# Kernel optimization log

Hardware: AMD Instinct MI355X
Metric: run time of the kernel (lower is better)

The kernel has to match this reference:

```python
import jax, jax.numpy as jnp
import numpy as np

NUM_TRAITS = 5
NUM_MODALITIES = 3
K = 8
EPS = 1e-08


def setup_inputs() -> dict:
    key = jax.random.key(0)
    k1, k2, k3, k4 = jax.random.split(key, 4)
    labeled_embeddings = jax.random.normal(k1, (20000, NUM_MODALITIES, 256), dtype=jnp.float32)
    labeled_traits = jax.random.uniform(k2, (20000, NUM_TRAITS), dtype=jnp.float32)
    unlabeled_embeddings = jax.random.normal(k3, (2048, NUM_MODALITIES, 256), dtype=jnp.float32)
    trait_modality_logits = jax.random.normal(k4, (NUM_TRAITS, NUM_MODALITIES), dtype=jnp.float32)
    return {
        'labeled_embeddings': labeled_embeddings,
        'labeled_traits': labeled_traits,
        'unlabeled_embeddings': unlabeled_embeddings,
        'trait_modality_logits': trait_modality_logits,
    }


def reference(labeled_embeddings, labeled_traits, unlabeled_embeddings, trait_modality_logits):
    # L2-normalize along feature dim (eps added to norm, matching torch code)
    lab_norm = labeled_embeddings / (jnp.linalg.norm(labeled_embeddings, axis=-1, keepdims=True) + EPS)
    unl_norm = unlabeled_embeddings / (jnp.linalg.norm(unlabeled_embeddings, axis=-1, keepdims=True) + EPS)

    # per-modality cosine similarity: [U, M, L]
    modality_sim = jnp.einsum('umd,lmd->uml', unl_norm, lab_norm)

    # per-trait modality weights and weighted similarity: [U, T, L]
    modality_weights = jax.nn.softmax(trait_modality_logits, axis=-1)  # [T, M]
    combined_sim = jnp.einsum('tm,uml->utl', modality_weights, modality_sim)

    # top-k neighbors per (query, trait)
    _, neighbor_indices = jax.lax.top_k(combined_sim, K)  # [U, T, K]

    # gather modality embeddings for neighbors: [U, T, K, M, D]
    neighbor_embeddings = labeled_embeddings[neighbor_indices]

    # gather the trait value corresponding to each trait head: [U, T, K]
    trait_ids = jnp.arange(NUM_TRAITS)[None, :, None]  # [1, T, 1]
    neighbor_traits = labeled_traits[neighbor_indices, trait_ids]

    return neighbor_embeddings, neighbor_traits, neighbor_indices.astype(jnp.int64)
```

## Files before the change

### kernel.cpp

```cpp
#include <hip/hip_runtime.h>
#include <hip/hip_bf16.h>
#include <math.h>

#define L_CNT 20000
#define U_CNT 2048
#define M_CNT 3
#define D_CNT 256
#define KTOT  768
#define T_CNT 5
#define K_OUT 8
#define KC    16
#define LP    20096
#define LROWS (L_CNT*M_CNT)
#define UROWS (U_CNT*M_CNT)
#define CHUNKS 313
#define CPAD   320

typedef unsigned short ushort_t;
typedef unsigned int uint_t;
typedef __attribute__((ext_vector_type(8))) short bf16x8;
typedef __attribute__((ext_vector_type(4))) float f32x4;

__device__ inline double dshfl_xor(double v, int m){
    long long x = __double_as_longlong(v);
    int lo = (int)(x & 0xffffffffLL);
    int hi = (int)(((unsigned long long)x) >> 32);
    lo = __shfl_xor(lo, m, 64);
    hi = __shfl_xor(hi, m, 64);
    return __longlong_as_double(((long long)hi << 32) | (long long)(unsigned int)lo);
}
__device__ inline unsigned short f2bf(float f){
    unsigned int u = __float_as_uint(f);
    u = (u + 0x7fffu + ((u >> 16) & 1u)) >> 16;
    return (unsigned short)u;
}
__device__ __forceinline__ void gload16(const void* g, void* l){
    __builtin_amdgcn_global_load_lds(
        (const __attribute__((address_space(1))) unsigned int*)g,
        (__attribute__((address_space(3))) unsigned int*)l, 16, 0, 0);
}
__device__ __forceinline__ float h2f(ushort_t h){
    _Float16 x; __builtin_memcpy(&x, &h, 2); return (float)x;
}
__device__ __forceinline__ ushort_t f2key(float f){
    _Float16 hv = (_Float16)f;
    ushort_t b; __builtin_memcpy(&b, &hv, 2);
    ushort_t mask = (ushort_t)(0x8000u | (((short)b >> 15) & 0x7FFF));
    return (ushort_t)(b ^ mask);
}
__device__ __forceinline__ ushort_t get16(const uint4& v, int e){
    uint_t w = (e < 2) ? v.x : (e < 4) ? v.y : (e < 6) ? v.z : v.w;
    return (ushort_t)((e & 1) ? (w >> 16) : (w & 0xFFFFu));
}
__device__ __forceinline__ float comb3(float w0, float w1, float w2, float a, float b, float c){
    return fmaf(w2, c, fmaf(w1, b, w0*a));
}
__device__ __forceinline__ void radix_find(uint_t hist[4][256], uint_t* h1, uint_t* h2,
    int tid, uint_t addBase, uint_t kc, uint_t* shB, uint_t* shAbove)
{
    h1[tid] = hist[0][tid]+hist[1][tid]+hist[2][tid]+hist[3][tid];
    uint_t* src = h1; uint_t* dst = h2;
    for (int st=1; st<256; st<<=1){
        __syncthreads();
        dst[tid] = src[tid] + ((tid+st < 256) ? src[tid+st] : 0u);
        uint_t* tt = src; src = dst; dst = tt;
    }
    __syncthreads();
    uint_t ge = src[tid] + addBase;
    uint_t gt = ((tid < 255) ? src[tid+1] : 0u) + addBase;
    if (ge >= kc && gt < kc){ *shB = (uint_t)tid; *shAbove = gt; }
    __syncthreads();
}

__global__ void weights_kernel(const float* __restrict__ logits,
                               float* __restrict__ w32, double* __restrict__ w64){
    int t = threadIdx.x;
    if (t < T_CNT){
        float a = logits[t*M_CNT+0], b = logits[t*M_CNT+1], c = logits[t*M_CNT+2];
        float mx = fmaxf(a, fmaxf(b, c));
        float e0 = expf(a-mx), e1 = expf(b-mx), e2 = expf(c-mx);
        float s = e0+e1+e2;
        w32[t*M_CNT+0] = e0/s; w32[t*M_CNT+1] = e1/s; w32[t*M_CNT+2] = e2/s;
        double da=(double)a, db=(double)b, dc=(double)c;
        double dmx = fmax(da, fmax(db, dc));
        double f0 = exp(da-dmx), f1 = exp(db-dmx), f2 = exp(dc-dmx);
        double ds = f0+f1+f2;
        w64[t*M_CNT+0] = f0/ds; w64[t*M_CNT+1] = f1/ds; w64[t*M_CNT+2] = f2/ds;
    }
}

__global__ __launch_bounds__(256) void prep_kernel(const float* __restrict__ lab,
    const float* __restrict__ unl, double* __restrict__ invL64, double* __restrict__ invU64,
    ushort_t* __restrict__ labN, ushort_t* __restrict__ unlN){
    const int NROW = LROWS + UROWS;
    int row = blockIdx.x*4 + (threadIdx.x >> 6);
    int lane = threadIdx.x & 63;
    if (row >= NROW) return;
    bool isLab = row < LROWS;
    const float* p = isLab ? (lab + (size_t)row*D_CNT) : (unl + (size_t)(row-LROWS)*D_CNT);
    float4 a = ((const float4*)p)[lane];
    double sS = (double)a.x*a.x + (double)a.y*a.y + (double)a.z*a.z + (double)a.w*a.w;
#pragma unroll
    for (int m=1;m<64;m<<=1) sS += dshfl_xor(sS, m);
    double inv = 1.0/(sqrt(sS) + 1e-8);
    if (lane == 0){
        if (isLab) invL64[row] = inv;
        else invU64[row-LROWS] = inv;
    }
    float sc = (float)inv;
    ushort4 o;
    o.x = f2bf(a.x*sc); o.y = f2bf(a.y*sc); o.z = f2bf(a.z*sc); o.w = f2bf(a.w*sc);
    ushort_t* dst = isLab ? (labN + (size_t)row*D_CNT) : (unlN + (size_t)(row-LROWS)*D_CNT);
    *(ushort4*)&dst[lane*4] = o;
}

__global__ __launch_bounds__(256) void sim_kernel(
    const ushort_t* __restrict__ labN, const ushort_t* __restrict__ unlN,
    ushort_t* __restrict__ slabp)
{
    __shared__ ushort_t sA[128][64];
    __shared__ ushort_t sB[128][64];
    __shared__ float    sT[64][132];

    const int tid  = threadIdx.x;
    const int lane = tid & 63;
    const int w    = tid >> 6;
    const int wu = w >> 1, wl = w & 1;
    const int fr = lane & 15, fg = lane >> 4;

    const int uB = blockIdx.x * 128;
    const int l0 = blockIdx.y * 128;

    const int sr   = lane >> 3;
    const int scol = ((lane & 7) ^ sr) * 8;
    const ushort_t* pA[4]; const ushort_t* pB[4];
    ushort_t* dA[4]; ushort_t* dB[4];
#pragma unroll
    for (int g=0; g<4; g++){
        int ar = uB + g*32 + w*8 + sr;
        pA[g] = unlN + (size_t)ar*KTOT + scol;
        dA[g] = &sA[g*32 + w*8][0];
        int br = l0 + g*32 + w*8 + sr; if (br > L_CNT-1) br = L_CNT-1;
        pB[g] = labN + (size_t)br*KTOT + scol;
        dB[g] = &sB[g*32 + w*8][0];
    }

    int aoff[4][2], boff[4][2];
#pragma unroll
    for (int i=0;i<4;i++)
#pragma unroll
        for (int ks=0;ks<2;ks++){
            int sw = ((ks*4 + fg) ^ (fr & 7)) * 16;
            aoff[i][ks] = (wu*64 + i*16 + fr)*128 + sw;
            boff[i][ks] = (wl*64 + i*16 + fr)*128 + sw;
        }

#pragma unroll
    for (int m=0; m<M_CNT; m++){
        f32x4 acc[4][4];
#pragma unroll
        for (int i=0;i<4;i++)
#pragma unroll
            for (int j=0;j<4;j++) acc[i][j] = (f32x4){0.f,0.f,0.f,0.f};

#pragma unroll
        for (int kb=0; kb<4; kb++){
            const int koff = (m*4 + kb) * 64;
            __syncthreads();
#pragma unroll
            for (int g=0; g<4; g++){
                gload16(pA[g] + koff, dA[g]);
                gload16(pB[g] + koff, dB[g]);
            }
            __syncthreads();
#pragma unroll
            for (int ks=0; ks<2; ks++){
                bf16x8 af[4], bf[4];
#pragma unroll
                for (int i=0;i<4;i++) af[i] = *(const bf16x8*)((const char*)sA + aoff[i][ks]);
#pragma unroll
                for (int j=0;j<4;j++) bf[j] = *(const bf16x8*)((const char*)sB + boff[j][ks]);
#pragma unroll
                for (int i=0;i<4;i++)
#pragma unroll
                    for (int j=0;j<4;j++)
                        acc[i][j] = __builtin_amdgcn_mfma_f32_16x16x32_bf16(af[i], bf[j], acc[i][j], 0, 0, 0);
            }
        }
#pragma unroll
        for (int half=0; half<2; half++){
            __syncthreads();
            if (wu == half){
#pragma unroll
                for (int i=0;i<4;i++)
#pragma unroll
                    for (int j=0;j<4;j++)
#pragma unroll
                        for (int r=0;r<4;r++)
                            sT[i*16 + fg*4 + r][wl*64 + j*16 + fr] = acc[i][j][r];
            }
            __syncthreads();
#pragma unroll
            for (int it=0; it<4; it++){
                int row = it*16 + (tid >> 4);
                int c0  = (tid & 15) * 8;
                ushort_t h[8];
#pragma unroll
                for (int e=0;e<8;e++){
                    _Float16 hv = (_Float16)sT[row][c0 + e];
                    __builtin_memcpy(&h[e], &hv, 2);
                }
                size_t base = ((size_t)(uB + half*64 + row)*M_CNT + m)*LP + l0 + c0;
                *(uint4*)&slabp[base] = *(const uint4*)h;
            }
        }
        __syncthreads();
    }
}

__global__ __launch_bounds__(256) void chunkmax_kernel(
    const ushort_t* __restrict__ slabp, const float* __restrict__ w32,
    ushort_t* __restrict__ chunkMax)
{
    __shared__ ushort_t cmax[T_CNT][CPAD];
    const int tid = threadIdx.x;
    const int u = blockIdx.x;

    float w[T_CNT][3];
#pragma unroll
    for (int t=0;t<T_CNT;t++)
#pragma unroll
        for (int m=0;m<3;m++) w[t][m] = w32[t*3+m];

    const uint4* p0 = (const uint4*)(slabp + ((size_t)u*M_CNT + 0)*LP);
    const uint4* p1 = (const uint4*)(slabp + ((size_t)u*M_CNT + 1)*LP);
    const uint4* p2 = (const uint4*)(slabp + ((size_t)u*M_CNT + 2)*LP);

    for (int i=tid; i<T_CNT*CPAD; i+=256) ((ushort_t*)cmax)[i] = 0;
    __syncthreads();

    for (int i=tid; i<2504; i+=256){
        uint_t km[T_CNT] = {0,0,0,0,0};
        if (i < 2500){
            uint4 x = p0[i], y = p1[i], z = p2[i];
            float a[8], b[8], c[8];
#pragma unroll
            for (int e=0;e<8;e++){
                a[e] = h2f(get16(x,e)); b[e] = h2f(get16(y,e)); c[e] = h2f(get16(z,e));
            }
#pragma unroll
            for (int t=0;t<T_CNT;t++){
                uint_t m = 0;
#pragma unroll
                for (int e=0;e<8;e++){
                    uint_t k = f2key(comb3(w[t][0],w[t][1],w[t][2], a[e],b[e],c[e]));
                    m = (k > m) ? k : m;
                }
                km[t] = m;
            }
        }
#pragma unroll
        for (int t=0;t<T_CNT;t++){
            uint_t k = km[t], o;
            o = __shfl_xor((int)k, 1, 64); k = ((uint_t)o > k) ? (uint_t)o : k;
            o = __shfl_xor((int)k, 2, 64); k = ((uint_t)o > k) ? (uint_t)o : k;
            o = __shfl_xor((int)k, 4, 64); k = ((uint_t)o > k) ? (uint_t)o : k;
            if ((tid & 7) == 0) cmax[t][i>>3] = (ushort_t)k;
        }
    }
    __syncthreads();
    for (int i=tid; i<T_CNT*CPAD; i+=256){
        int t = i / CPAD, c = i % CPAD;
        chunkMax[((size_t)u*T_CNT + t)*CPAD + c] = cmax[t][c];
    }
}

__global__ __launch_bounds__(256) void select2_kernel(
    const ushort_t* __restrict__ slabp, const ushort_t* __restrict__ chunkMax,
    const float* __restrict__ w32, int* __restrict__ candIdx)
{
    __shared__ ushort_t mxs[CPAD];
    __shared__ ushort_t cand[CPAD];
    __shared__ uint_t hist[4][256];
    __shared__ uint_t h1[256], h2[256];
    __shared__ uint_t shB, shAbove, shNc, shCtr0, shCtr1;
    __shared__ int bufc[KC];

    const int tid = threadIdx.x, wid = tid >> 6;
    const int u = blockIdx.x, t = blockIdx.y;
    const float w0 = w32[t*3+0], w1 = w32[t*3+1], w2 = w32[t*3+2];
    const ushort_t* s0 = slabp + ((size_t)u*M_CNT + 0)*LP;
    const ushort_t* s1 = slabp + ((size_t)u*M_CNT + 1)*LP;
    const ushort_t* s2 = slabp + ((size_t)u*M_CNT + 2)*LP;
    const ushort_t* cm = chunkMax + ((size_t)u*T_CNT + t)*CPAD;

    for (int i=tid; i<CPAD; i+=256) mxs[i] = (i < CHUNKS) ? cm[i] : (ushort_t)0;
    hist[0][tid]=0; hist[1][tid]=0; hist[2][tid]=0; hist[3][tid]=0;
    if (tid == 0){ shNc = 0; shCtr0 = 0; shCtr1 = 0; }
    __syncthreads();

    for (int i=tid; i<CHUNKS; i+=256) atomicAdd(&hist[wid][mxs[i] >> 8], 1u);
    __syncthreads();
    radix_find(hist, h1, h2, tid, 0u, KC, &shB, &shAbove);
    const uint_t MB = shB, mAb = shAbove;
    hist[0][tid]=0; hist[1][tid]=0; hist[2][tid]=0; hist[3][tid]=0;
    __syncthreads();
    for (int i=tid; i<CHUNKS; i+=256){
        uint_t k = mxs[i];
        if ((k >> 8) == MB) atomicAdd(&hist[wid][k & 0xFFu], 1u);
    }
    __syncthreads();
    radix_find(hist, h1, h2, tid, mAb, KC, &shB, &shAbove);
    const uint_t tau = (MB << 8) | shB;
    hist[0][tid]=0; hist[1][tid]=0; hist[2][tid]=0; hist[3][tid]=0;
    __syncthreads();

    for (int i=tid; i<CHUNKS; i+=256)
        if ((uint_t)mxs[i] >= tau) cand[atomicAdd(&shNc, 1u)] = (ushort_t)i;
    __syncthreads();
    const int NE = (int)shNc * 64;

    for (int j=tid; j<NE; j+=256){
        int l = (int)cand[j>>6]*64 + (j & 63);
        if (l < L_CNT){
            uint_t k = f2key(comb3(w0,w1,w2, h2f(s0[l]), h2f(s1[l]), h2f(s2[l])));
            atomicAdd(&hist[wid][k >> 8], 1u);
        }
    }
    __syncthreads();
    radix_find(hist, h1, h2, tid, 0u, KC, &shB, &shAbove);
    const uint_t EB = shB, eAb = shAbove;
    hist[0][tid]=0; hist[1][tid]=0; hist[2][tid]=0; hist[3][tid]=0;
    __syncthreads();

    for (int j=tid; j<NE; j+=256){
        int l = (int)cand[j>>6]*64 + (j & 63);
        if (l < L_CNT){
            uint_t k = f2key(comb3(w0,w1,w2, h2f(s0[l]), h2f(s1[l]), h2f(s2[l])));
            if ((k >> 8) == EB) atomicAdd(&hist[wid][k & 0xFFu], 1u);
        }
    }
    __syncthreads();
    radix_find(hist, h1, h2, tid, eAb, KC, &shB, &shAbove);
    const uint_t K16 = (EB << 8) | shB;
    const uint_t tot = shAbove;

    for (int j=tid; j<NE; j+=256){
        int l = (int)cand[j>>6]*64 + (j & 63);
        if (l < L_CNT){
            uint_t k = f2key(comb3(w0,w1,w2, h2f(s0[l]), h2f(s1[l]), h2f(s2[l])));
            if (k > K16){
                bufc[atomicAdd(&shCtr0, 1u)] = l;
            } else if (k == K16){
                uint_t s = atomicAdd(&shCtr1, 1u) + tot;
                if (s < (uint_t)KC) bufc[s] = l;
            }
        }
    }
    __syncthreads();
    if (tid < KC) candIdx[((size_t)u*T_CNT + t)*KC + tid] = bufc[tid];
}

__global__ __launch_bounds__(256) void rescore_kernel(
    const float* __restrict__ lab, const float* __restrict__ unl,
    const double* __restrict__ w64, const double* __restrict__ invL64,
    const double* __restrict__ invU64, const int* __restrict__ candIdx,
    double* __restrict__ candSim)
{
    int q = blockIdx.x*4 + (threadIdx.x >> 6);
    int lane = threadIdx.x & 63;
    int ut = q >> 4;
    int t = ut % T_CNT;
    int u = ut / T_CNT;
    int idx = candIdx[q];
    double sim = 0.0;
#pragma unroll
    for (int m=0;m<M_CNT;m++){
        float4 a = *(const float4*)&unl[(((size_t)u*M_CNT)+m)*D_CNT + lane*4];
        float4 b = *(const float4*)&lab[(((size_t)idx*M_CNT)+m)*D_CNT + lane*4];
        double d = (double)a.x*b.x + (double)a.y*b.y + (double)a.z*b.z + (double)a.w*b.w;
#pragma unroll
        for (int mm=1;mm<64;mm<<=1) d += dshfl_xor(d, mm);
        sim += w64[t*M_CNT+m] * d * invU64[u*M_CNT+m] * invL64[idx*M_CNT+m];
    }
    if (lane == 0) candSim[q] = sim;
}

__global__ __launch_bounds__(256) void finalize_kernel(
    const double* __restrict__ candSim, const int* __restrict__ candIdx,
    const float* __restrict__ traits,
    float* __restrict__ outTraits, float* __restrict__ outIdx, int* __restrict__ finalIdx)
{
    int id = blockIdx.x*256 + threadIdx.x;
    if (id >= U_CNT*T_CNT) return;
    int t = id % T_CNT;
    double cv[KC]; int ci[KC];
#pragma unroll
    for (int c=0;c<KC;c++){ cv[c] = candSim[(size_t)id*KC + c]; ci[c] = candIdx[(size_t)id*KC + c]; }
#pragma unroll
    for (int i=0;i<KC;i++)
#pragma unroll
        for (int j=0;j<KC-1;j++){
            bool sw = (cv[j] < cv[j+1]) || (cv[j] == cv[j+1] && ci[j] > ci[j+1]);
            if (sw){ double tv=cv[j]; cv[j]=cv[j+1]; cv[j+1]=tv; int ti=ci[j]; ci[j]=ci[j+1]; ci[j+1]=ti; }
        }
#pragma unroll
    for (int k=0;k<K_OUT;k++){
        size_t ob = (size_t)id*K_OUT + k;
        int fi = ci[k];
        outTraits[ob] = traits[(size_t)fi*T_CNT + t];
        outIdx[ob] = (float)fi;
        finalIdx[ob] = fi;
    }
}

__global__ __launch_bounds__(192) void gather_kernel(const float* __restrict__ lab,
    const int* __restrict__ finalIdx, float* __restrict__ outEmb)
{
    int b = blockIdx.x;
    int idx = finalIdx[b];
    const float4* src = (const float4*)(lab + (size_t)idx * (M_CNT*D_CNT));
    float4* dst = (float4*)(outEmb + (size_t)b * (M_CNT*D_CNT));
    dst[threadIdx.x] = src[threadIdx.x];
}

extern "C" void kernel_launch(void* const* d_in, const int* in_sizes, int n_in,
                              void* d_out, int out_size, void* d_ws, size_t ws_size,
                              hipStream_t stream) {
    const float* lab    = (const float*)d_in[0];
    const float* traits = (const float*)d_in[1];
    const float* unl    = (const float*)d_in[2];
    const float* logits = (const float*)d_in[3];

    float* out = (float*)d_out;
    float* outEmb = out;
    float* outTr  = out + (size_t)U_CNT*T_CNT*K_OUT*M_CNT*D_CNT;
    float* outIx  = outTr + (size_t)U_CNT*T_CNT*K_OUT;

    char* wsb = (char*)d_ws;
    size_t off = 0;
    auto take = [&](size_t bytes)->void*{
        void* p = wsb + off;
        off = (off + bytes + 255) & ~(size_t)255;
        return p;
    };
    double* invL64 = (double*)take((size_t)LROWS*sizeof(double));
    double* invU64 = (double*)take((size_t)UROWS*sizeof(double));
    float*  w32    = (float*) take(T_CNT*M_CNT*sizeof(float));
    double* w64    = (double*)take(T_CNT*M_CNT*sizeof(double));
    int*    candIdx= (int*)   take((size_t)U_CNT*T_CNT*KC*sizeof(int));
    double* candSim= (double*)take((size_t)U_CNT*T_CNT*KC*sizeof(double));
    int*    finalIdx=(int*)   take((size_t)U_CNT*T_CNT*K_OUT*sizeof(int));
    ushort_t* labN = (ushort_t*)take((size_t)LROWS*D_CNT*sizeof(ushort_t));
    ushort_t* unlN = (ushort_t*)take((size_t)UROWS*D_CNT*sizeof(ushort_t));
    ushort_t* chunkMax = (ushort_t*)take((size_t)U_CNT*T_CNT*CPAD*sizeof(ushort_t));

    ushort_t* slabV = (ushort_t*)outEmb;

    weights_kernel<<<1, 64, 0, stream>>>(logits, w32, w64);
    {
        int nrow = LROWS + UROWS;
        prep_kernel<<<(nrow+3)/4, 256, 0, stream>>>(lab, unl, invL64, invU64, labN, unlN);
    }
    sim_kernel<<<dim3(U_CNT/128, (L_CNT + 127)/128), 256, 0, stream>>>(labN, unlN, slabV);
    chunkmax_kernel<<<U_CNT, 256, 0, stream>>>(slabV, w32, chunkMax);
    select2_kernel<<<dim3(U_CNT, T_CNT), 256, 0, stream>>>(slabV, chunkMax, w32, candIdx);
    rescore_kernel<<<(U_CNT*T_CNT*KC)/4, 256, 0, stream>>>(lab, unl, w64, invL64, invU64, candIdx, candSim);
    finalize_kernel<<<(U_CNT*T_CNT + 255)/256, 256, 0, stream>>>(candSim, candIdx, traits, outTr, outIx, finalIdx);
    gather_kernel<<<U_CNT*T_CNT*K_OUT, 192, 0, stream>>>(lab, finalIdx, outEmb);
}
```

Before: 416.8 us.

## Fuse per-chunk max computation into similarity GEMM epilogue

The separate chunkmax kernel, which re-read the whole fp16 similarity slab from memory, is removed. Its work now runs in the sim kernel's epilogue, which keeps the m=0 and m=1 fp16 tiles in registers and computes the per-trait chunk maxima when the m=2 tile is written. Launch bounds are also raised to request two blocks per CU. The cost is higher register pressure from the held tiles and extra epilogue ALU work, which could hurt occupancy or cause spills.

```diff
diff --git a/kernel.cpp b/kernel.cpp
--- a/kernel.cpp
+++ b/kernel.cpp
@@ -114,9 +114,10 @@
     *(ushort4*)&dst[lane*4] = o;
 }
 
-__global__ __launch_bounds__(256) void sim_kernel(
+__global__ __launch_bounds__(256, 2) void sim_kernel(
     const ushort_t* __restrict__ labN, const ushort_t* __restrict__ unlN,
-    ushort_t* __restrict__ slabp)
+    const float* __restrict__ w32, ushort_t* __restrict__ slabp,
+    ushort_t* __restrict__ chunkMax)
 {
     __shared__ ushort_t sA[128][64];
     __shared__ ushort_t sB[128][64];
@@ -155,6 +156,8 @@
             boff[i][ks] = (wl*64 + i*16 + fr)*128 + sw;
         }
 
+    uint4 hA[2][4], hB[2][4];
+
 #pragma unroll
     for (int m=0; m<M_CNT; m++){
         f32x4 acc[4][4];
@@ -187,6 +190,15 @@
                         acc[i][j] = __builtin_amdgcn_mfma_f32_16x16x32_bf16(af[i], bf[j], acc[i][j], 0, 0, 0);
             }
         }
+
+        float wl5[T_CNT][3];
+        if (m == 2){
+#pragma unroll
+            for (int t=0;t<T_CNT;t++)
+#pragma unroll
+                for (int j=0;j<3;j++) wl5[t][j] = w32[t*3+j];
+        }
+
 #pragma unroll
         for (int half=0; half<2; half++){
             __syncthreads();
@@ -200,78 +212,59 @@
                             sT[i*16 + fg*4 + r][wl*64 + j*16 + fr] = acc[i][j][r];
             }
             __syncthreads();
+            const int c0 = (tid & 15) * 8;
 #pragma unroll
             for (int it=0; it<4; it++){
                 int row = it*16 + (tid >> 4);
-                int c0  = (tid & 15) * 8;
                 ushort_t h[8];
 #pragma unroll
                 for (int e=0;e<8;e++){
-                    _Float16 hv = (_Float16)sT[row][c0 + e];
-                    __builtin_memcpy(&h[e], &hv, 2);
+                    _Float16 hv16 = (_Float16)sT[row][c0 + e];
+                    __builtin_memcpy(&h[e], &hv16, 2);
                 }
+                uint4 hv = *(const uint4*)h;
                 size_t base = ((size_t)(uB + half*64 + row)*M_CNT + m)*LP + l0 + c0;
-                *(uint4*)&slabp[base] = *(const uint4*)h;
+                *(uint4*)&slabp[base] = hv;
+
+                if (m == 0) hA[half][it] = hv;
+                else if (m == 1) hB[half][it] = hv;
+                else {
+                    uint_t rm[T_CNT] = {0,0,0,0,0};
+#pragma unroll
+                    for (int e=0;e<8;e++){
+                        int l = l0 + c0 + e;
+                        float a = h2f(get16(hA[half][it], e));
+                        float b = h2f(get16(hB[half][it], e));
+                        float c = h2f(get16(hv, e));
+                        if (l < L_CNT){
+#pragma unroll
+                            for (int t=0;t<T_CNT;t++){
+                                uint_t k = f2key(comb3(wl5[t][0],wl5[t][1],wl5[t][2], a,b,c));
+                                rm[t] = (k > rm[t]) ? k : rm[t];
+                            }
+                        }
+                    }
+#pragma unroll
+                    for (int t=0;t<T_CNT;t++){
+                        uint_t k = rm[t], o;
+                        o = (uint_t)__shfl_xor((int)k, 1, 64); k = (o > k) ? o : k;
+                        o = (uint_t)__shfl_xor((int)k, 2, 64); k = (o > k) ? o : k;
+                        o = (uint_t)__shfl_xor((int)k, 4, 64); k = (o > k) ? o : k;
+                        rm[t] = k;
+                    }
+                    if ((tid & 7) == 0){
+                        int chunkc = (l0 >> 6) + ((tid >> 3) & 1);
+                        if (chunkc < CHUNKS){
+                            int ug = uB + half*64 + row;
+#pragma unroll
+                            for (int t=0;t<T_CNT;t++)
+                                chunkMax[((size_t)ug*T_CNT + t)*CPAD + chunkc] = (ushort_t)rm[t];
+                        }
+                    }
+                }
             }
         }
         __syncthreads();
-    }
-}
-
-__global__ __launch_bounds__(256) void chunkmax_kernel(
-    const ushort_t* __restrict__ slabp, const float* __restrict__ w32,
-    ushort_t* __restrict__ chunkMax)
-{
-    __shared__ ushort_t cmax[T_CNT][CPAD];
-    const int tid = threadIdx.x;
-    const int u = blockIdx.x;
-
-    float w[T_CNT][3];
-#pragma unroll
-    for (int t=0;t<T_CNT;t++)
-#pragma unroll
-        for (int m=0;m<3;m++) w[t][m] = w32[t*3+m];
-
-    const uint4* p0 = (const uint4*)(slabp + ((size_t)u*M_CNT + 0)*LP);
-    const uint4* p1 = (const uint4*)(slabp + ((size_t)u*M_CNT + 1)*LP);
-    const uint4* p2 = (const uint4*)(slabp + ((size_t)u*M_CNT + 2)*LP);
-
-    for (int i=tid; i<T_CNT*CPAD; i+=256) ((ushort_t*)cmax)[i] = 0;
-    __syncthreads();
-
-    for (int i=tid; i<2504; i+=256){
-        uint_t km[T_CNT] = {0,0,0,0,0};
-        if (i < 2500){
-            uint4 x = p0[i], y = p1[i], z = p2[i];
-            float a[8], b[8], c[8];
-#pragma unroll
-            for (int e=0;e<8;e++){
-                a[e] = h2f(get16(x,e)); b[e] = h2f(get16(y,e)); c[e] = h2f(get16(z,e));
-            }
-#pragma unroll
-            for (int t=0;t<T_CNT;t++){
-                uint_t m = 0;
-#pragma unroll
-                for (int e=0;e<8;e++){
-                    uint_t k = f2key(comb3(w[t][0],w[t][1],w[t][2], a[e],b[e],c[e]));
-                    m = (k > m) ? k : m;
-                }
-                km[t] = m;
-            }
-        }
-#pragma unroll
-        for (int t=0;t<T_CNT;t++){
-            uint_t k = km[t], o;
-            o = __shfl_xor((int)k, 1, 64); k = ((uint_t)o > k) ? (uint_t)o : k;
-            o = __shfl_xor((int)k, 2, 64); k = ((uint_t)o > k) ? (uint_t)o : k;
-            o = __shfl_xor((int)k, 4, 64); k = ((uint_t)o > k) ? (uint_t)o : k;
-            if ((tid & 7) == 0) cmax[t][i>>3] = (ushort_t)k;
-        }
-    }
-    __syncthreads();
-    for (int i=tid; i<T_CNT*CPAD; i+=256){
-        int t = i / CPAD, c = i % CPAD;
-        chunkMax[((size_t)u*T_CNT + t)*CPAD + c] = cmax[t][c];
     }
 }
 
@@ -462,8 +455,7 @@
         int nrow = LROWS + UROWS;
         prep_kernel<<<(nrow+3)/4, 256, 0, stream>>>(lab, unl, invL64, invU64, labN, unlN);
     }
-    sim_kernel<<<dim3(U_CNT/128, (L_CNT + 127)/128), 256, 0, stream>>>(labN, unlN, slabV);
-    chunkmax_kernel<<<U_CNT, 256, 0, stream>>>(slabV, w32, chunkMax);
+    sim_kernel<<<dim3(U_CNT/128, (L_CNT + 127)/128), 256, 0, stream>>>(labN, unlN, w32, slabV, chunkMax);
     select2_kernel<<<dim3(U_CNT, T_CNT), 256, 0, stream>>>(slabV, chunkMax, w32, candIdx);
     rescore_kernel<<<(U_CNT*T_CNT*KC)/4, 256, 0, stream>>>(lab, unl, w64, invL64, invU64, candIdx, candSim);
     finalize_kernel<<<(U_CNT*T_CNT + 255)/256, 256, 0, stream>>>(candSim, candIdx, traits, outTr, outIx, finalIdx);
```

Result: no change. 414.4 us (-0.6%).
